# Optimization experiments

Measured on AMD Instinct MI355X. Metric: run time of the kernel, lower is better.

The kernel has to match this reference:

```python
import jax, jax.numpy as jnp
import numpy as np

W, L, D = 4096, 32, 256
WORD_VOCAB, CHR_VOCAB = 50000, 128


def conv1d(x, w, b):
    # x: [N, C_in, T], w: [C_out, C_in, 3], padding=1 (same)
    y = jax.lax.conv_general_dilated(
        x, w, window_strides=(1,), padding=[(1, 1)],
        dimension_numbers=("NCW", "OIW", "NCW"))
    return y + b[None, :, None]


def setup_inputs() -> dict:
    key = jax.random.key(0)
    ks = jax.random.split(key, 12)
    words = jax.random.randint(ks[0], (W,), 0, WORD_VOCAB, dtype=jnp.int32)
    words_in_char = jax.random.randint(ks[1], (W, L), 0, CHR_VOCAB, dtype=jnp.int32)
    s = 0.02
    word_emb = (jax.random.normal(ks[2], (WORD_VOCAB, D), jnp.float32) * s).at[0].set(0.0)  # padding_idx=0
    chr_emb = (jax.random.normal(ks[3], (CHR_VOCAB, D), jnp.float32) * s).at[0].set(0.0)
    conv_chr_w = jax.random.normal(ks[4], (D, D, 3), jnp.float32) * s
    conv_chr_b = jax.random.normal(ks[5], (D,), jnp.float32) * s
    conv_sent_w = jax.random.normal(ks[6], (2 * D, 2 * D, 3), jnp.float32) * s
    conv_sent_b = jax.random.normal(ks[7], (2 * D,), jnp.float32) * s
    w1 = jax.random.normal(ks[8], (4 * D, 2 * D), jnp.float32) * s
    b1 = jax.random.normal(ks[9], (4 * D,), jnp.float32) * s
    w2 = jax.random.normal(ks[10], (2, 4 * D), jnp.float32) * s
    b2 = jax.random.normal(ks[11], (2,), jnp.float32) * s
    return dict(words=words, words_in_char=words_in_char,
                word_emb=word_emb, chr_emb=chr_emb,
                conv_chr_w=conv_chr_w, conv_chr_b=conv_chr_b,
                conv_sent_w=conv_sent_w, conv_sent_b=conv_sent_b,
                w1=w1, b1=b1, w2=w2, b2=b2)


def reference(words, words_in_char, word_emb, chr_emb,
              conv_chr_w, conv_chr_b, conv_sent_w, conv_sent_b,
              w1, b1, w2, b2):
    # word embeddings: [W, D]
    vector_wrds = word_emb[words]
    # char path, batched over all words (equivalent to the per-word loop):
    ch = chr_emb[words_in_char]                      # [W, L, D]
    ch = jnp.transpose(ch, (0, 2, 1))                # [W, D, L]
    wc = conv1d(ch, conv_chr_w, conv_chr_b)          # [W, D, L]
    vector_wchs = jnp.max(wc, axis=2)                # [W, D]
    # sentence conv over the word axis
    u = jnp.concatenate([vector_wrds, vector_wchs], axis=1)  # [W, 2D]
    u = u.T[None, :, :]                              # [1, 2D, W]
    r = conv1d(u, conv_sent_w, conv_sent_b)          # [1, 2D, W]
    r = jnp.max(r, axis=2)                           # [1, 2D]
    h = jnp.tanh(r @ w1.T + b1)                      # [1, 4D]
    return h @ w2.T + b2                             # [1, 2]
```

## Files before the change

### kernel.cpp

```cpp
#include <hip/hip_runtime.h>
#include <hip/hip_bf16.h>
#include <math.h>

#define NW 4096
#define NL 32
#define ND 256
#define ND2 512
#define ND4 1024

typedef __attribute__((ext_vector_type(8))) short short8;
typedef __attribute__((ext_vector_type(4))) float floatx4;


__global__ __launch_bounds__(256) void transpose_chr_w(
    const float* __restrict__ src, float* __restrict__ dst) {
  int idx = blockIdx.x * 256 + threadIdx.x;
  float v = src[idx];
  int co = idx / 768;
  int rem = idx - co * 768;
  int ci = rem / 3;
  int k = rem - ci * 3;
  dst[k * 65536 + ci * 256 + co] = v;
}

__global__ __launch_bounds__(256) void transpose_sent_w_bf16(
    const float* __restrict__ src, __hip_bfloat16* __restrict__ dst) {
  int idx = blockIdx.x * 256 + threadIdx.x;
  float v = src[idx];
  int co = idx / 1536;
  int rem = idx - co * 1536;
  int ci = rem / 3;
  int k = rem - ci * 3;
  dst[k * 262144 + co * 512 + ci] = __float2bfloat16(v);
}

__global__ __launch_bounds__(1024) void zero_guard(__hip_bfloat16* __restrict__ u_base) {
  int tid = threadIdx.x;
  if (tid < 512) u_base[tid] = __float2bfloat16(0.f);
  else           u_base[4097 * 512 + (tid - 512)] = __float2bfloat16(0.f);
}

__global__ __launch_bounds__(256) void table_kernel(
    const float* __restrict__ chr_emb, const float* __restrict__ wT,
    float* __restrict__ T) {
  __shared__ float s_e[256];
  int k = blockIdx.x >> 7;
  int c = blockIdx.x & 127;
  int co = threadIdx.x;
  s_e[co] = chr_emb[c * 256 + co];
  __syncthreads();
  const float* wk = wT + k * 65536;
  float acc = 0.f;
#pragma unroll 8
  for (int ci = 0; ci < 256; ++ci)
    acc = fmaf(s_e[ci], wk[ci * 256 + co], acc);
  T[(k * 128 + c) * 256 + co] = acc;
}

__global__ __launch_bounds__(256) void char_word_kernel(
    const int* __restrict__ words, const int* __restrict__ wic,
    const float* __restrict__ word_emb, const float* __restrict__ T,
    const float* __restrict__ bias, __hip_bfloat16* __restrict__ u0) {
  __shared__ int s_ch[NL];
  int w = blockIdx.x;
  int co = threadIdx.x;
  if (co < NL) s_ch[co] = wic[w * NL + co];
  __syncthreads();
  int wid = words[w];
  u0[w * ND2 + co] = __float2bfloat16(word_emb[wid * ND + co]);
  const float* T0 = T;
  const float* T1 = T + 32768;
  const float* T2 = T + 65536;
  float m = -INFINITY;
#pragma unroll
  for (int t = 0; t < NL; ++t) {
    float s = T1[s_ch[t] * ND + co];
    if (t > 0)      s += T0[s_ch[t - 1] * ND + co];
    if (t < NL - 1) s += T2[s_ch[t + 1] * ND + co];
    m = fmaxf(m, s);
  }
  u0[w * ND2 + ND + co] = __float2bfloat16(m + bias[co]);
}

__global__ __launch_bounds__(256) void sent_conv_mfma(
    const __hip_bfloat16* __restrict__ u0,
    const __hip_bfloat16* __restrict__ Wb,
    float* __restrict__ partial) {
  __shared__ short As[64][64];
  __shared__ short Bs[64][64];
  __shared__ float sm[4][32];
  const int tid = threadIdx.x;
  const int t0 = blockIdx.x * 64;
  const int co0 = blockIdx.y * 64;
  const int wave = tid >> 6;
  const int lane = tid & 63;
  const int wy = wave >> 1, wx = wave & 1;
  const int m = lane & 15, q = lane >> 4;

  floatx4 acc[2][2];
#pragma unroll
  for (int i = 0; i < 2; ++i)
#pragma unroll
    for (int j = 0; j < 2; ++j) acc[i][j] = (floatx4){0.f, 0.f, 0.f, 0.f};

  const int srow = tid >> 3;
  const int sch  = tid & 7;

  for (int k = 0; k < 3; ++k) {
    const short* WbK = (const short*)Wb + k * 262144 + co0 * 512;
    const short* uK  = (const short*)u0 + (t0 + k - 1) * 512;
    for (int ci0 = 0; ci0 < 512; ci0 += 64) {
#pragma unroll
      for (int r = 0; r < 2; ++r) {
        int row = srow + r * 32;
        *(uint4*)&As[row][sch * 8] = *(const uint4*)(WbK + row * 512 + ci0 + sch * 8);
        *(uint4*)&Bs[row][sch * 8] = *(const uint4*)(uK  + row * 512 + ci0 + sch * 8);
      }
      __syncthreads();
#pragma unroll
      for (int kk = 0; kk < 2; ++kk) {
        short8 a0 = *(const short8*)&As[wy * 32 + m][kk * 32 + q * 8];
        short8 a1 = *(const short8*)&As[wy * 32 + 16 + m][kk * 32 + q * 8];
        short8 b0 = *(const short8*)&Bs[wx * 32 + m][kk * 32 + q * 8];
        short8 b1 = *(const short8*)&Bs[wx * 32 + 16 + m][kk * 32 + q * 8];
        acc[0][0] = __builtin_amdgcn_mfma_f32_16x16x32_bf16(a0, b0, acc[0][0], 0, 0, 0);
        acc[0][1] = __builtin_amdgcn_mfma_f32_16x16x32_bf16(a0, b1, acc[0][1], 0, 0, 0);
        acc[1][0] = __builtin_amdgcn_mfma_f32_16x16x32_bf16(a1, b0, acc[1][0], 0, 0, 0);
        acc[1][1] = __builtin_amdgcn_mfma_f32_16x16x32_bf16(a1, b1, acc[1][1], 0, 0, 0);
      }
      __syncthreads();
    }
  }

#pragma unroll
  for (int i = 0; i < 2; ++i)
#pragma unroll
    for (int r = 0; r < 4; ++r) {
      float x = fmaxf(acc[i][0][r], acc[i][1][r]);
#pragma unroll
      for (int off = 1; off < 16; off <<= 1)
        x = fmaxf(x, __shfl_xor(x, off, 64));
      if (m == 0) sm[wave][i * 16 + q * 4 + r] = x;
    }
  __syncthreads();
  if (tid < 64) {
    int whalf = tid >> 5;
    float v = fmaxf(sm[whalf * 2 + 0][tid & 31], sm[whalf * 2 + 1][tid & 31]);
    partial[(co0 + tid) * 64 + blockIdx.x] = v;
  }
}

__global__ __launch_bounds__(512) void reduce_r(
    const float* __restrict__ partial, const float* __restrict__ bs,
    float* __restrict__ r) {
  int tid = threadIdx.x;
  const float4* p = (const float4*)(partial + tid * 64);
  float m = -INFINITY;
#pragma unroll
  for (int j = 0; j < 16; ++j) {
    float4 v = p[j];
    m = fmaxf(m, fmaxf(fmaxf(v.x, v.y), fmaxf(v.z, v.w)));
  }
  r[tid] = m + bs[tid];
}

__global__ __launch_bounds__(256) void fc1_kernel(
    const float* __restrict__ r, const float* __restrict__ w1,
    const float* __restrict__ b1, float* __restrict__ h) {
  int wave = threadIdx.x >> 6;
  int lane = threadIdx.x & 63;
  int o = blockIdx.x * 4 + wave;
  const float4* wv = (const float4*)(w1 + o * 512 + lane * 8);
  const float4* rv = (const float4*)(r + lane * 8);
  float4 w0 = wv[0], w1v = wv[1];
  float4 r0 = rv[0], r1 = rv[1];
  float acc = w0.x * r0.x + w0.y * r0.y + w0.z * r0.z + w0.w * r0.w +
              w1v.x * r1.x + w1v.y * r1.y + w1v.z * r1.z + w1v.w * r1.w;
#pragma unroll
  for (int off = 32; off >= 1; off >>= 1) acc += __shfl_down(acc, off, 64);
  if (lane == 0) h[o] = tanhf(acc + b1[o]);
}

__global__ __launch_bounds__(128) void fc2_kernel(
    const float* __restrict__ h, const float* __restrict__ w2,
    const float* __restrict__ b2, float* __restrict__ out) {
  int tid = threadIdx.x;
  int o = tid >> 6;
  int lane = tid & 63;
  float acc = 0.f;
#pragma unroll
  for (int j = 0; j < 16; ++j)
    acc = fmaf(w2[o * 1024 + lane + j * 64], h[lane + j * 64], acc);
#pragma unroll
  for (int off = 32; off >= 1; off >>= 1) acc += __shfl_down(acc, off, 64);
  if (lane == 0) out[o] = acc + b2[o];
}

extern "C" void kernel_launch(void* const* d_in, const int* in_sizes, int n_in,
                              void* d_out, int out_size, void* d_ws, size_t ws_size,
                              hipStream_t stream) {
  const int*   words       = (const int*)d_in[0];
  const int*   wic         = (const int*)d_in[1];
  const float* word_emb    = (const float*)d_in[2];
  const float* chr_emb     = (const float*)d_in[3];
  const float* conv_chr_w  = (const float*)d_in[4];
  const float* conv_chr_b  = (const float*)d_in[5];
  const float* conv_sent_w = (const float*)d_in[6];
  const float* conv_sent_b = (const float*)d_in[7];
  const float* w1          = (const float*)d_in[8];
  const float* b1          = (const float*)d_in[9];
  const float* w2          = (const float*)d_in[10];
  const float* b2          = (const float*)d_in[11];
  float* out = (float*)d_out;

  float* ws     = (float*)d_ws;
  float* T_buf  = ws;
  float* wT_buf = T_buf + 98304;
  float* part   = wT_buf + 196608;
  float* r_buf  = part + 32768;
  float* h_buf  = r_buf + 512;
  __hip_bfloat16* u_base = (__hip_bfloat16*)(h_buf + 1024);
  __hip_bfloat16* u0     = u_base + 512;
  __hip_bfloat16* Wb     = u_base + 4098 * 512;

  transpose_chr_w<<<768, 256, 0, stream>>>(conv_chr_w, wT_buf);
  transpose_sent_w_bf16<<<3072, 256, 0, stream>>>(conv_sent_w, Wb);
  zero_guard<<<1, 1024, 0, stream>>>(u_base);
  table_kernel<<<384, 256, 0, stream>>>(chr_emb, wT_buf, T_buf);
  char_word_kernel<<<4096, 256, 0, stream>>>(words, wic, word_emb, T_buf,
                                             conv_chr_b, u0);
  sent_conv_mfma<<<dim3(64, 8), 256, 0, stream>>>(u0, Wb, part);
  reduce_r<<<1, 512, 0, stream>>>(part, conv_sent_b, r_buf);
  fc1_kernel<<<256, 256, 0, stream>>>(r_buf, w1, b1, h_buf);
  fc2_kernel<<<1, 128, 0, stream>>>(h_buf, w2, b2, out);
}
```

Measured before the change: 182.4 us.

## Fuse prep kernels, tile char conv in LDS with bf16 table, widen sentence GEMM tiles

Merges the weight transposes and guard zeroing into one prep kernel, and moves the word-embedding gather into its own kernel. The character lookup table is stored in bf16 and tiled by output-channel group so each block holds it in LDS and processes 64 words. The sentence conv GEMM gets 128-row tiles, an XOR-swizzled LDS layout and register prefetch of the next k-slice, and the max-reduce is folded into fc1. The bf16 table adds rounding error to the char path, and prep_kernel's word-gather branch is never reached because it is launched with exactly 3841 blocks.

```diff
diff --git a/kernel.cpp b/kernel.cpp
--- a/kernel.cpp
+++ b/kernel.cpp
@@ -6,172 +6,254 @@
 #define NL 32
 #define ND 256
 #define ND2 512
-#define ND4 1024
 
 typedef __attribute__((ext_vector_type(8))) short short8;
 typedef __attribute__((ext_vector_type(4))) float floatx4;
 
-
-__global__ __launch_bounds__(256) void transpose_chr_w(
-    const float* __restrict__ src, float* __restrict__ dst) {
+__device__ inline float bfval(short s) {
+  union { unsigned u; float f; } v;
+  v.u = ((unsigned)(unsigned short)s) << 16;
+  return v.f;
+}
+
+
+__global__ __launch_bounds__(256) void prep_kernel(
+    const float* __restrict__ conv_sent_w, const float* __restrict__ conv_chr_w,
+    const int* __restrict__ words, const float* __restrict__ word_emb,
+    float* __restrict__ wT, __hip_bfloat16* __restrict__ Wb,
+    short* __restrict__ u_base) {
+  int b = blockIdx.x;
+  int tid = threadIdx.x;
+  if (b < 3072) {
+    int idx = b * 256 + tid;
+    float v = conv_sent_w[idx];
+    int co = idx / 1536;
+    int rem = idx - co * 1536;
+    int ci = rem / 3;
+    int k = rem - ci * 3;
+    Wb[k * 262144 + co * 512 + ci] = __float2bfloat16(v);
+  } else if (b < 3840) {
+    int idx = (b - 3072) * 256 + tid;
+    float v = conv_chr_w[idx];
+    int co = idx / 768;
+    int rem = idx - co * 768;
+    int ci = rem / 3;
+    int k = rem - ci * 3;
+    wT[k * 65536 + ci * 256 + co] = v;
+  } else if (b == 3840) {
+    u_base[tid] = 0;
+    u_base[tid + 256] = 0;
+    u_base[4097 * 512 + tid] = 0;
+    u_base[4097 * 512 + tid + 256] = 0;
+  } else {
+    int idx = (b - 3841) * 256 + tid;
+    int w = idx >> 8;
+    int co = idx & 255;
+    int wid = words[w];
+    u_base[512 + w * 512 + co] =
+        ((short*)&((unsigned&)word_emb[wid * 256 + co]))[1];
+  }
+}
+
+__global__ __launch_bounds__(256) void word_gather_kernel(
+    const int* __restrict__ words, const float* __restrict__ word_emb,
+    __hip_bfloat16* __restrict__ u0) {
   int idx = blockIdx.x * 256 + threadIdx.x;
-  float v = src[idx];
-  int co = idx / 768;
-  int rem = idx - co * 768;
-  int ci = rem / 3;
-  int k = rem - ci * 3;
-  dst[k * 65536 + ci * 256 + co] = v;
-}
-
-__global__ __launch_bounds__(256) void transpose_sent_w_bf16(
-    const float* __restrict__ src, __hip_bfloat16* __restrict__ dst) {
-  int idx = blockIdx.x * 256 + threadIdx.x;
-  float v = src[idx];
-  int co = idx / 1536;
-  int rem = idx - co * 1536;
-  int ci = rem / 3;
-  int k = rem - ci * 3;
-  dst[k * 262144 + co * 512 + ci] = __float2bfloat16(v);
-}
-
-__global__ __launch_bounds__(1024) void zero_guard(__hip_bfloat16* __restrict__ u_base) {
-  int tid = threadIdx.x;
-  if (tid < 512) u_base[tid] = __float2bfloat16(0.f);
-  else           u_base[4097 * 512 + (tid - 512)] = __float2bfloat16(0.f);
+  int w = idx >> 8;
+  int co = idx & 255;
+  int wid = words[w];
+  u0[w * 512 + co] = __float2bfloat16(word_emb[wid * 256 + co]);
 }
 
 __global__ __launch_bounds__(256) void table_kernel(
     const float* __restrict__ chr_emb, const float* __restrict__ wT,
-    float* __restrict__ T) {
-  __shared__ float s_e[256];
-  int k = blockIdx.x >> 7;
-  int c = blockIdx.x & 127;
+    __hip_bfloat16* __restrict__ Tb) {
+  __shared__ float s_e[4][256];
+  int k = blockIdx.x >> 5;
+  int c0 = (blockIdx.x & 31) * 4;
   int co = threadIdx.x;
-  s_e[co] = chr_emb[c * 256 + co];
+#pragma unroll
+  for (int j = 0; j < 4; ++j) s_e[j][co] = chr_emb[(c0 + j) * 256 + co];
   __syncthreads();
   const float* wk = wT + k * 65536;
-  float acc = 0.f;
+  float a0 = 0.f, a1 = 0.f, a2 = 0.f, a3 = 0.f;
 #pragma unroll 8
-  for (int ci = 0; ci < 256; ++ci)
-    acc = fmaf(s_e[ci], wk[ci * 256 + co], acc);
-  T[(k * 128 + c) * 256 + co] = acc;
+  for (int ci = 0; ci < 256; ++ci) {
+    float w = wk[ci * 256 + co];
+    a0 = fmaf(s_e[0][ci], w, a0);
+    a1 = fmaf(s_e[1][ci], w, a1);
+    a2 = fmaf(s_e[2][ci], w, a2);
+    a3 = fmaf(s_e[3][ci], w, a3);
+  }
+  int base = ((co >> 6) * 3 + k) * 8192 + (co & 63);
+  Tb[base + (c0 + 0) * 64] = __float2bfloat16(a0);
+  Tb[base + (c0 + 1) * 64] = __float2bfloat16(a1);
+  Tb[base + (c0 + 2) * 64] = __float2bfloat16(a2);
+  Tb[base + (c0 + 3) * 64] = __float2bfloat16(a3);
 }
 
 __global__ __launch_bounds__(256) void char_word_kernel(
-    const int* __restrict__ words, const int* __restrict__ wic,
-    const float* __restrict__ word_emb, const float* __restrict__ T,
+    const int* __restrict__ wic, const __hip_bfloat16* __restrict__ Tb,
     const float* __restrict__ bias, __hip_bfloat16* __restrict__ u0) {
-  __shared__ int s_ch[NL];
-  int w = blockIdx.x;
-  int co = threadIdx.x;
-  if (co < NL) s_ch[co] = wic[w * NL + co];
+  __shared__ short sT[3 * 128 * 64];
+  __shared__ int s_wic[64 * 32];
+  int ct = blockIdx.x >> 6;
+  int w0 = (blockIdx.x & 63) * 64;
+  int tid = threadIdx.x;
+  {
+    const uint4* src = (const uint4*)((const short*)Tb + ct * 24576);
+    uint4* dst = (uint4*)sT;
+#pragma unroll
+    for (int i = 0; i < 12; ++i) dst[tid + i * 256] = src[tid + i * 256];
+    const int4* wsrc = (const int4*)(wic + w0 * 32);
+    int4* wdst = (int4*)s_wic;
+    wdst[tid] = wsrc[tid];
+    wdst[tid + 256] = wsrc[tid + 256];
+  }
   __syncthreads();
-  int wid = words[w];
-  u0[w * ND2 + co] = __float2bfloat16(word_emb[wid * ND + co]);
-  const float* T0 = T;
-  const float* T1 = T + 32768;
-  const float* T2 = T + 65536;
-  float m = -INFINITY;
-#pragma unroll
-  for (int t = 0; t < NL; ++t) {
-    float s = T1[s_ch[t] * ND + co];
-    if (t > 0)      s += T0[s_ch[t - 1] * ND + co];
-    if (t < NL - 1) s += T2[s_ch[t + 1] * ND + co];
-    m = fmaxf(m, s);
-  }
-  u0[w * ND2 + ND + co] = __float2bfloat16(m + bias[co]);
+  int co_l = tid & 63;
+  int slot = tid >> 6;
+  float bb = bias[ct * 64 + co_l];
+  const short* T0 = sT;
+  const short* T1 = sT + 8192;
+  const short* T2 = sT + 16384;
+  for (int wi = 0; wi < 16; ++wi) {
+    int wl = slot * 16 + wi;
+    const int* ch = s_wic + wl * 32;
+    float m = -INFINITY;
+#pragma unroll
+    for (int t = 0; t < NL; ++t) {
+      float s = bfval(T1[ch[t] * 64 + co_l]);
+      if (t > 0) s += bfval(T0[ch[t - 1] * 64 + co_l]);
+      if (t < NL - 1) s += bfval(T2[ch[t + 1] * 64 + co_l]);
+      m = fmaxf(m, s);
+    }
+    u0[(w0 + wl) * ND2 + ND + ct * 64 + co_l] = __float2bfloat16(m + bb);
+  }
 }
 
 __global__ __launch_bounds__(256) void sent_conv_mfma(
     const __hip_bfloat16* __restrict__ u0,
     const __hip_bfloat16* __restrict__ Wb,
     float* __restrict__ partial) {
-  __shared__ short As[64][64];
-  __shared__ short Bs[64][64];
-  __shared__ float sm[4][32];
+  __shared__ short As[128 * 64];
+  __shared__ short Bs[64 * 64];
+  __shared__ float sm[2][128];
   const int tid = threadIdx.x;
   const int t0 = blockIdx.x * 64;
-  const int co0 = blockIdx.y * 64;
-  const int wave = tid >> 6;
-  const int lane = tid & 63;
+  const int co0 = blockIdx.y * 128;
+  const int wave = tid >> 6, lane = tid & 63;
   const int wy = wave >> 1, wx = wave & 1;
   const int m = lane & 15, q = lane >> 4;
 
-  floatx4 acc[2][2];
-#pragma unroll
-  for (int i = 0; i < 2; ++i)
+  floatx4 acc[4][2];
+#pragma unroll
+  for (int i = 0; i < 4; ++i)
 #pragma unroll
     for (int j = 0; j < 2; ++j) acc[i][j] = (floatx4){0.f, 0.f, 0.f, 0.f};
 
-  const int srow = tid >> 3;
-  const int sch  = tid & 7;
-
-  for (int k = 0; k < 3; ++k) {
-    const short* WbK = (const short*)Wb + k * 262144 + co0 * 512;
-    const short* uK  = (const short*)u0 + (t0 + k - 1) * 512;
-    for (int ci0 = 0; ci0 < 512; ci0 += 64) {
-#pragma unroll
-      for (int r = 0; r < 2; ++r) {
-        int row = srow + r * 32;
-        *(uint4*)&As[row][sch * 8] = *(const uint4*)(WbK + row * 512 + ci0 + sch * 8);
-        *(uint4*)&Bs[row][sch * 8] = *(const uint4*)(uK  + row * 512 + ci0 + sch * 8);
+  int aoff[2][4], boff[2][2];
+#pragma unroll
+  for (int kk = 0; kk < 2; ++kk) {
+#pragma unroll
+    for (int i = 0; i < 4; ++i) {
+      int row = wy * 64 + i * 16 + m;
+      aoff[kk][i] = row * 64 + (((kk * 4 + q) ^ (row & 7)) * 8);
+    }
+#pragma unroll
+    for (int j = 0; j < 2; ++j) {
+      int row = wx * 32 + j * 16 + m;
+      boff[kk][j] = row * 64 + (((kk * 4 + q) ^ (row & 7)) * 8);
+    }
+  }
+
+  const int sc = tid & 7, sr = tid >> 3;
+  const int swc = (sc ^ (sr & 7)) * 8;
+  const short* WbS = (const short*)Wb;
+  const short* uS = (const short*)u0;
+
+  uint4 pa[4], pb[2];
+  {
+    const short* WbK = WbS;
+    const short* uK = uS + (t0 - 1) * 512;
+#pragma unroll
+    for (int ii = 0; ii < 4; ++ii)
+      pa[ii] = *(const uint4*)(WbK + (co0 + sr + ii * 32) * 512 + sc * 8);
+#pragma unroll
+    for (int ii = 0; ii < 2; ++ii)
+      pb[ii] = *(const uint4*)(uK + (sr + ii * 32) * 512 + sc * 8);
+  }
+
+  for (int s = 0; s < 24; ++s) {
+#pragma unroll
+    for (int ii = 0; ii < 4; ++ii)
+      *(uint4*)&As[(sr + ii * 32) * 64 + swc] = pa[ii];
+#pragma unroll
+    for (int ii = 0; ii < 2; ++ii)
+      *(uint4*)&Bs[(sr + ii * 32) * 64 + swc] = pb[ii];
+    __syncthreads();
+    if (s + 1 < 24) {
+      int sn = s + 1;
+      int k = sn >> 3, ci0 = (sn & 7) << 6;
+      const short* WbK = WbS + k * 262144;
+      const short* uK = uS + (t0 + k - 1) * 512;
+#pragma unroll
+      for (int ii = 0; ii < 4; ++ii)
+        pa[ii] = *(const uint4*)(WbK + (co0 + sr + ii * 32) * 512 + ci0 + sc * 8);
+#pragma unroll
+      for (int ii = 0; ii < 2; ++ii)
+        pb[ii] = *(const uint4*)(uK + (sr + ii * 32) * 512 + ci0 + sc * 8);
+    }
+#pragma unroll
+    for (int kk = 0; kk < 2; ++kk) {
+      short8 b0 = *(const short8*)&Bs[boff[kk][0]];
+      short8 b1 = *(const short8*)&Bs[boff[kk][1]];
+#pragma unroll
+      for (int i = 0; i < 4; ++i) {
+        short8 a = *(const short8*)&As[aoff[kk][i]];
+        acc[i][0] = __builtin_amdgcn_mfma_f32_16x16x32_bf16(a, b0, acc[i][0], 0, 0, 0);
+        acc[i][1] = __builtin_amdgcn_mfma_f32_16x16x32_bf16(a, b1, acc[i][1], 0, 0, 0);
       }
-      __syncthreads();
-#pragma unroll
-      for (int kk = 0; kk < 2; ++kk) {
-        short8 a0 = *(const short8*)&As[wy * 32 + m][kk * 32 + q * 8];
-        short8 a1 = *(const short8*)&As[wy * 32 + 16 + m][kk * 32 + q * 8];
-        short8 b0 = *(const short8*)&Bs[wx * 32 + m][kk * 32 + q * 8];
-        short8 b1 = *(const short8*)&Bs[wx * 32 + 16 + m][kk * 32 + q * 8];
-        acc[0][0] = __builtin_amdgcn_mfma_f32_16x16x32_bf16(a0, b0, acc[0][0], 0, 0, 0);
-        acc[0][1] = __builtin_amdgcn_mfma_f32_16x16x32_bf16(a0, b1, acc[0][1], 0, 0, 0);
-        acc[1][0] = __builtin_amdgcn_mfma_f32_16x16x32_bf16(a1, b0, acc[1][0], 0, 0, 0);
-        acc[1][1] = __builtin_amdgcn_mfma_f32_16x16x32_bf16(a1, b1, acc[1][1], 0, 0, 0);
-      }
-      __syncthreads();
-    }
-  }
-
-#pragma unroll
-  for (int i = 0; i < 2; ++i)
+    }
+    __syncthreads();
+  }
+
+#pragma unroll
+  for (int i = 0; i < 4; ++i)
 #pragma unroll
     for (int r = 0; r < 4; ++r) {
       float x = fmaxf(acc[i][0][r], acc[i][1][r]);
 #pragma unroll
       for (int off = 1; off < 16; off <<= 1)
         x = fmaxf(x, __shfl_xor(x, off, 64));
-      if (m == 0) sm[wave][i * 16 + q * 4 + r] = x;
+      if (m == 0) sm[wx][wy * 64 + i * 16 + q * 4 + r] = x;
     }
   __syncthreads();
-  if (tid < 64) {
-    int whalf = tid >> 5;
-    float v = fmaxf(sm[whalf * 2 + 0][tid & 31], sm[whalf * 2 + 1][tid & 31]);
-    partial[(co0 + tid) * 64 + blockIdx.x] = v;
-  }
-}
-
-__global__ __launch_bounds__(512) void reduce_r(
+  if (tid < 128)
+    partial[(co0 + tid) * 64 + blockIdx.x] = fmaxf(sm[0][tid], sm[1][tid]);
+}
+
+__global__ __launch_bounds__(512) void fc1_kernel(
     const float* __restrict__ partial, const float* __restrict__ bs,
-    float* __restrict__ r) {
+    const float* __restrict__ w1, const float* __restrict__ b1,
+    float* __restrict__ h) {
+  __shared__ float s_r[512];
   int tid = threadIdx.x;
-  const float4* p = (const float4*)(partial + tid * 64);
-  float m = -INFINITY;
-#pragma unroll
-  for (int j = 0; j < 16; ++j) {
-    float4 v = p[j];
-    m = fmaxf(m, fmaxf(fmaxf(v.x, v.y), fmaxf(v.z, v.w)));
-  }
-  r[tid] = m + bs[tid];
-}
-
-__global__ __launch_bounds__(256) void fc1_kernel(
-    const float* __restrict__ r, const float* __restrict__ w1,
-    const float* __restrict__ b1, float* __restrict__ h) {
-  int wave = threadIdx.x >> 6;
-  int lane = threadIdx.x & 63;
-  int o = blockIdx.x * 4 + wave;
+  {
+    const float4* p = (const float4*)(partial + tid * 64);
+    float mm = -INFINITY;
+#pragma unroll
+    for (int j = 0; j < 16; ++j) {
+      float4 v = p[j];
+      mm = fmaxf(mm, fmaxf(fmaxf(v.x, v.y), fmaxf(v.z, v.w)));
+    }
+    s_r[tid] = mm + bs[tid];
+  }
+  __syncthreads();
+  int wave = tid >> 6, lane = tid & 63;
+  int o = blockIdx.x * 8 + wave;
   const float4* wv = (const float4*)(w1 + o * 512 + lane * 8);
-  const float4* rv = (const float4*)(r + lane * 8);
+  const float4* rv = (const float4*)(s_r + lane * 8);
   float4 w0 = wv[0], w1v = wv[1];
   float4 r0 = rv[0], r1 = rv[1];
   float acc = w0.x * r0.x + w0.y * r0.y + w0.z * r0.z + w0.w * r0.w +
@@ -213,24 +295,22 @@
   const float* b2          = (const float*)d_in[11];
   float* out = (float*)d_out;
 
-  float* ws     = (float*)d_ws;
-  float* T_buf  = ws;
-  float* wT_buf = T_buf + 98304;
-  float* part   = wT_buf + 196608;
-  float* r_buf  = part + 32768;
-  float* h_buf  = r_buf + 512;
-  __hip_bfloat16* u_base = (__hip_bfloat16*)(h_buf + 1024);
-  __hip_bfloat16* u0     = u_base + 512;
-  __hip_bfloat16* Wb     = u_base + 4098 * 512;
-
-  transpose_chr_w<<<768, 256, 0, stream>>>(conv_chr_w, wT_buf);
-  transpose_sent_w_bf16<<<3072, 256, 0, stream>>>(conv_sent_w, Wb);
-  zero_guard<<<1, 1024, 0, stream>>>(u_base);
-  table_kernel<<<384, 256, 0, stream>>>(chr_emb, wT_buf, T_buf);
-  char_word_kernel<<<4096, 256, 0, stream>>>(words, wic, word_emb, T_buf,
-                                             conv_chr_b, u0);
-  sent_conv_mfma<<<dim3(64, 8), 256, 0, stream>>>(u0, Wb, part);
-  reduce_r<<<1, 512, 0, stream>>>(part, conv_sent_b, r_buf);
-  fc1_kernel<<<256, 256, 0, stream>>>(r_buf, w1, b1, h_buf);
+  float* ws    = (float*)d_ws;
+  float* wT    = ws;
+  float* part  = wT + 196608;
+  float* h_buf = part + 32768;
+  short* Tb    = (short*)(h_buf + 1024);
+  short* u_base = Tb + 98304;
+  __hip_bfloat16* u0 = (__hip_bfloat16*)(u_base + 512);
+  __hip_bfloat16* Wb = (__hip_bfloat16*)(u_base + 4098 * 512);
+
+  prep_kernel<<<3841, 256, 0, stream>>>(conv_sent_w, conv_chr_w, words,
+                                        word_emb, wT, Wb, u_base);
+  word_gather_kernel<<<4096, 256, 0, stream>>>(words, word_emb, u0);
+  table_kernel<<<96, 256, 0, stream>>>(chr_emb, wT, (__hip_bfloat16*)Tb);
+  char_word_kernel<<<256, 256, 0, stream>>>(wic, (const __hip_bfloat16*)Tb,
+                                            conv_chr_b, u0);
+  sent_conv_mfma<<<dim3(64, 4), 256, 0, stream>>>(u0, Wb, part);
+  fc1_kernel<<<128, 512, 0, stream>>>(part, conv_sent_b, w1, b1, h_buf);
   fc2_kernel<<<1, 128, 0, stream>>>(h_buf, w2, b2, out);
 }
```

Measured after the change: 220.5 us. 20.8% more time.
